# Kernel tuning notes

Hardware: AMD Instinct MI355X
Metric: run time of the kernel (lower is better)

Reference implementation:

```python
import jax, jax.numpy as jnp
import numpy as np

T, B, XD, HD, ZD = 256, 512, 64, 512, 32
EPS_C = 1e-5  # EPS in the torch source

SHAPES = {
    "x": (T, B, XD), "eps": (T, B, ZD),
    "phi_x_W1": (HD, XD), "phi_x_b1": (HD,), "phi_x_W2": (HD, HD), "phi_x_b2": (HD,),
    "phi_z_W": (HD, ZD), "phi_z_b": (HD,),
    "enc_W1": (HD, 2 * HD), "enc_b1": (HD,), "enc_W2": (HD, HD), "enc_b2": (HD,),
    "enc_mean_W": (ZD, HD), "enc_mean_b": (ZD,), "enc_std_W": (ZD, HD), "enc_std_b": (ZD,),
    "prior_W": (HD, HD), "prior_b": (HD,),
    "prior_mean_W": (ZD, HD), "prior_mean_b": (ZD,), "prior_std_W": (ZD, HD), "prior_std_b": (ZD,),
    "dec_W1": (HD, 2 * HD), "dec_b1": (HD,), "dec_W2": (HD, HD), "dec_b2": (HD,),
    "dec_std_W": (XD, HD), "dec_std_b": (XD,),
    "dec_mean_W1": (XD, HD), "dec_mean_b1": (XD,), "dec_mean_W2": (XD, XD), "dec_mean_b2": (XD,),
    "gru_Wih": (3 * HD, 2 * HD), "gru_Whh": (3 * HD, HD),
}

def setup_inputs() -> dict:
    key = jax.random.key(0)
    out = {}
    for i, (name, shp) in enumerate(SHAPES.items()):
        scale = 1.0 if name in ("x", "eps") else 0.05
        out[name] = jax.random.normal(jax.random.fold_in(key, i), shp, jnp.float32) * scale
    return out

def _lin(x, W, b):
    return x @ W.T + b

def _vrnn(x, eps, p):
    relu, softplus, sigmoid = jax.nn.relu, jax.nn.softplus, jax.nn.sigmoid
    h0 = jnp.zeros((x.shape[1], HD), x.dtype)  # n_layers = 1

    def step(h, xe):
        xt, et = xe  # [B, XD], [B, ZD]
        phi_x = relu(_lin(relu(_lin(xt, p["phi_x_W1"], p["phi_x_b1"])), p["phi_x_W2"], p["phi_x_b2"]))
        enc_h = relu(_lin(relu(_lin(jnp.concatenate([phi_x, h], 1), p["enc_W1"], p["enc_b1"])), p["enc_W2"], p["enc_b2"]))
        enc_mean = _lin(enc_h, p["enc_mean_W"], p["enc_mean_b"])
        enc_std = softplus(_lin(enc_h, p["enc_std_W"], p["enc_std_b"]))
        prior_h = relu(_lin(h, p["prior_W"], p["prior_b"]))
        prior_mean = _lin(prior_h, p["prior_mean_W"], p["prior_mean_b"])
        prior_std = softplus(_lin(prior_h, p["prior_std_W"], p["prior_std_b"]))
        z = et * enc_std + enc_mean  # reparameterized sample with pre-drawn eps
        z = z.at[:, :4].multiply(10.0)  # _modify_z(modify_dims=[0,1,2,3], scale=10, shift=0)
        phi_z = relu(_lin(z, p["phi_z_W"], p["phi_z_b"]))
        dec_h = relu(_lin(relu(_lin(jnp.concatenate([phi_z, h], 1), p["dec_W1"], p["dec_b1"])), p["dec_W2"], p["dec_b2"]))
        dec_mean = _lin(relu(_lin(dec_h, p["dec_mean_W1"], p["dec_mean_b1"])), p["dec_mean_W2"], p["dec_mean_b2"])
        dec_std = softplus(_lin(dec_h, p["dec_std_W"], p["dec_std_b"]))
        # single-layer GRU cell, no bias (PyTorch gate order: r, z, n)
        gx = jnp.concatenate([phi_x, phi_z], 1) @ p["gru_Wih"].T
        gh = h @ p["gru_Whh"].T
        xr, xz, xn = jnp.split(gx, 3, 1)
        hr, hz, hn = jnp.split(gh, 3, 1)
        r = sigmoid(xr + hr)
        zg = sigmoid(xz + hz)
        n = jnp.tanh(xn + r * hn)
        h_new = (1.0 - zg) * n + zg * h
        s1 = jnp.maximum(enc_std, 1e-9)
        s2 = jnp.maximum(prior_std, 1e-9)
        kld = 0.5 * jnp.sum(jnp.log(s2 ** 2 / s1 ** 2) + (s1 ** 2 + (enc_mean - prior_mean) ** 2) / s2 ** 2 - 1.0)
        nll = jnp.sum(jnp.log(dec_std + EPS_C) + jnp.log(2.0 * jnp.pi) / 2.0 + (xt - dec_mean) ** 2 / (2.0 * dec_std ** 2))
        return h_new, (dec_mean, kld, nll)

    _, (dec_means, klds, nlls) = jax.lax.scan(step, h0, (x, eps))
    rec_loss = jnp.sum((dec_means - x) ** 2)  # F.mse_loss(..., reduction='sum')
    return rec_loss, jnp.sum(klds), jnp.sum(nlls), dec_means

def reference(x, eps, phi_x_W1, phi_x_b1, phi_x_W2, phi_x_b2, phi_z_W, phi_z_b, enc_W1, enc_b1, enc_W2, enc_b2, enc_mean_W, enc_mean_b, enc_std_W, enc_std_b, prior_W, prior_b, prior_mean_W, prior_mean_b, prior_std_W, prior_std_b, dec_W1, dec_b1, dec_W2, dec_b2, dec_std_W, dec_std_b, dec_mean_W1, dec_mean_b1, dec_mean_W2, dec_mean_b2, gru_Wih, gru_Whh):
    args = dict(locals())
    xv = args.pop("x")
    ev = args.pop("eps")
    return _vrnn(xv, ev, args)
```

## Files before the change

kernel.cpp:

```cpp
#include <hip/hip_runtime.h>
#include <hip/hip_bf16.h>
#include <math.h>


typedef __attribute__((ext_vector_type(8))) short bfrag;
typedef __attribute__((ext_vector_type(4))) short sfrag;
typedef __attribute__((ext_vector_type(4))) float ffrag;
typedef __hip_bfloat16 bf16;

__device__ __forceinline__ float softplus_f(float v) {
    return (v > 20.f) ? v : log1pf(expf(v));
}
__device__ __forceinline__ float sigmoid_f(float v) {
    return 1.f / (1.f + expf(-v));
}
__device__ __forceinline__ float s2f(short s) {
    union { unsigned u; float f; } c;
    c.u = ((unsigned)(unsigned short)s) << 16;
    return c.f;
}

__global__ __launch_bounds__(256) void f2b_kernel(
    const float* __restrict__ s, bf16* __restrict__ d, int n)
{
    int i = blockIdx.x * 256 + threadIdx.x;
    if (i < n) d[i] = __float2bfloat16(s[i]);
}
__global__ __launch_bounds__(256) void fcopy_kernel(
    const float* __restrict__ s, float* __restrict__ d, int n)
{
    int i = blockIdx.x * 256 + threadIdx.x;
    if (i < n) d[i] = s[i];
}

__global__ __launch_bounds__(256) void packw_kernel(
    const float* __restrict__ src, bf16* __restrict__ dst,
    int ldw, int n0, int k0, int KB, int total)
{
    int i = blockIdx.x * 256 + threadIdx.x;
    if (i >= total) return;
    const int j = i & 7;
    const int L = (i >> 3) & 63;
    const int r = i >> 9;
    const int kb = r % KB, t = r / KB;
    dst[i] = __float2bfloat16(
        src[(size_t)(n0 + t * 16 + (L & 15)) * ldw + k0 + kb * 32 + ((L >> 4) * 8) + j]);
}

__global__ __launch_bounds__(256) void init_kernel(
    float* __restrict__ hlive, bf16* __restrict__ hh0, float* __restrict__ out)
{
    const int idx = blockIdx.x * 256 + threadIdx.x;
    if (idx < 262144) { hlive[idx] = 0.f; hh0[idx] = __float2bfloat16(0.f); }
    if (idx < 3) out[idx] = 0.f;
}

__global__ __launch_bounds__(256) void gemm_p(
    const bf16* __restrict__ A0, int lda0, const bf16* __restrict__ W0p, int K0,
    const bf16* __restrict__ A1, int lda1, const bf16* __restrict__ W1p, int K1,
    const float* __restrict__ bias, int act,
    void* __restrict__ C, int ldc, int obf)
{
    __shared__ __align__(16) bf16 As[2][64][72];
    const int tid = threadIdx.x;
    const int L = tid & 63, w = tid >> 6;
    const int m0 = blockIdx.y * 64;
    const int n0 = blockIdx.x * 64;
    const int lr = L & 15, lk = (L >> 4) * 8;
    const int msub = (w & 1) * 32, nsub = (w >> 1) * 32;
    const int srow = tid >> 2, scol = (tid & 3) * 16;
    const size_t Lo = (size_t)L * 8;

    ffrag acc[2][2];
#pragma unroll
    for (int i = 0; i < 2; ++i)
#pragma unroll
        for (int j = 0; j < 2; ++j)
#pragma unroll
            for (int r = 0; r < 4; ++r) acc[i][j][r] = 0.f;

    for (int s = 0; s < 2; ++s) {
        const bf16* A = s ? A1 : A0;
        if (!A) break;
        const bf16* Wp = s ? W1p : W0p;
        const int lda = s ? lda1 : lda0;
        const int K   = s ? K1 : K0;
        const int KB = K >> 5;
        const int NP = K >> 6;
        const size_t t0 = (size_t)((n0 + nsub) >> 4);

        {
            const bf16* ap = A + (size_t)(m0 + srow) * lda + scol;
            *(bfrag*)&As[0][srow][scol]     = *(const bfrag*)(ap);
            *(bfrag*)&As[0][srow][scol + 8] = *(const bfrag*)(ap + 8);
        }
        __syncthreads();

        for (int kp = 0; kp < NP; ++kp) {
            if (kp + 1 < NP) {
                const bf16* ap = A + (size_t)(m0 + srow) * lda + (kp + 1) * 64 + scol;
                bf16* dst = &As[(kp + 1) & 1][srow][scol];
                *(bfrag*)(dst)     = *(const bfrag*)(ap);
                *(bfrag*)(dst + 8) = *(const bfrag*)(ap + 8);
            }
#pragma unroll
            for (int kbi = 0; kbi < 2; ++kbi) {
                const int kb = kp * 2 + kbi;
                bfrag b0 = *(const bfrag*)(Wp + ((t0 * KB + kb) << 9) + Lo);
                bfrag b1 = *(const bfrag*)(Wp + (((t0 + 1) * KB + kb) << 9) + Lo);
                bfrag a0 = *(const bfrag*)&As[kp & 1][msub + lr][kbi * 32 + lk];
                bfrag a1 = *(const bfrag*)&As[kp & 1][msub + 16 + lr][kbi * 32 + lk];
                acc[0][0] = __builtin_amdgcn_mfma_f32_16x16x32_bf16(a0, b0, acc[0][0], 0, 0, 0);
                acc[0][1] = __builtin_amdgcn_mfma_f32_16x16x32_bf16(a0, b1, acc[0][1], 0, 0, 0);
                acc[1][0] = __builtin_amdgcn_mfma_f32_16x16x32_bf16(a1, b0, acc[1][0], 0, 0, 0);
                acc[1][1] = __builtin_amdgcn_mfma_f32_16x16x32_bf16(a1, b1, acc[1][1], 0, 0, 0);
            }
            __syncthreads();
        }
    }

#pragma unroll
    for (int i = 0; i < 2; ++i)
#pragma unroll
    for (int j = 0; j < 2; ++j)
#pragma unroll
    for (int r = 0; r < 4; ++r) {
        const int row = m0 + msub + 16 * i + (L >> 4) * 4 + r;
        const int col = n0 + nsub + 16 * j + lr;
        float v = acc[i][j][r];
        if (bias) v += bias[col];
        if (act == 1) v = fmaxf(v, 0.f);
        else if (act == 2) { if (col >= 32) v = softplus_f(v); }
        else if (act == 3) { if (col < 64) v = fmaxf(v, 0.f); }
        if (obf == 1) {
            ((bf16*)C)[(size_t)row * ldc + col] = __float2bfloat16(v);
        } else if (obf == 2) {
            ((bf16*)C)[((size_t)(row >> 4) * (ldc >> 4) + (col >> 4)) * 256
                       + (size_t)L * 4 + r] = __float2bfloat16(v);
        } else {
            ((float*)C)[(size_t)row * ldc + col] = v;
        }
    }
}

#define AST 536

__global__ __launch_bounds__(512, 1) void encmid_kernel(
    const bf16* __restrict__ e1xp,
    const float* __restrict__ eps_c,
    const bf16* __restrict__ ew1hp,
    const bf16* __restrict__ ew2p,
    const float* __restrict__ eb2,
    const bf16* __restrict__ mswp,
    const float* __restrict__ msb,
    const bf16* __restrict__ pzwp,
    const float* __restrict__ pzb,
    bf16* __restrict__ hh,
    float* __restrict__ emsc,
    bf16* __restrict__ phizc,
    bf16* __restrict__ pzp,
    bf16* __restrict__ hpp,
    int lt, int hsrc0)
{
    __shared__ __align__(16) bf16 hB[16][AST];
    __shared__ __align__(16) bf16 p1[16][AST];
    __shared__ __align__(16) bf16 p2[16][AST];
    __shared__ float msd[16][65];
    __shared__ __align__(16) bf16 zb[16][40];

    const int tid = threadIdx.x;
    const int L = tid & 63, w = tid >> 6;
    const int lr = L & 15, lk = (L >> 4) * 8;
    const int rq = (L >> 4) * 4;
    const int bm = blockIdx.x;
    const int m0 = bm * 16;

    const int hrow = tid >> 5, hc0 = (tid & 31) * 16;
    const size_t Lo = (size_t)L * 8;

    const size_t rb = (size_t)lt * 512 + m0;
    const size_t rt = (size_t)lt * 32 + bm;

    {
        const int slot = (lt == 0) ? hsrc0 : lt;
        const bf16* hsv = hh + (size_t)slot * 262144 + (size_t)(m0 + hrow) * 512 + hc0;
        bfrag h0 = *(const bfrag*)(hsv);
        bfrag h1 = *(const bfrag*)(hsv + 8);
        *(bfrag*)&hB[hrow][hc0]     = h0;
        *(bfrag*)&hB[hrow][hc0 + 8] = h1;
        if (lt == 0 && hsrc0 != 0) {
            bf16* d0 = hh + (size_t)(m0 + hrow) * 512 + hc0;
            *(bfrag*)(d0)     = h0;
            *(bfrag*)(d0 + 8) = h1;
        }
    }
    __syncthreads();

#pragma unroll
    for (int q = 0; q < 2; ++q) {
        const int kb = w * 2 + q;
        *(bfrag*)(hpp + (((size_t)bm * 16 + kb) << 9) + Lo) =
            *(const bfrag*)&hB[lr][kb * 32 + lk];
    }

    {
        sfrag exv[4];
#pragma unroll
        for (int nt = 0; nt < 4; ++nt)
            exv[nt] = *(const sfrag*)(e1xp + (rt * 32 + 4 * w + nt) * 256 + (size_t)L * 4);

        bfrag wf[4][4];
#pragma unroll
        for (int d = 0; d < 4; ++d)
#pragma unroll
            for (int nt = 0; nt < 4; ++nt)
                wf[d][nt] = *(const bfrag*)(ew1hp + (((4 * w + nt) * 16 + d) << 9) + Lo);

        ffrag acc[4];
#pragma unroll
        for (int nt = 0; nt < 4; ++nt)
#pragma unroll
            for (int r = 0; r < 4; ++r) acc[nt][r] = 0.f;

#pragma unroll
        for (int kb = 0; kb < 16; ++kb) {
            bfrag a = *(const bfrag*)&hB[lr][kb * 32 + lk];
            const int cur = kb & 3;
#pragma unroll
            for (int nt = 0; nt < 4; ++nt)
                acc[nt] = __builtin_amdgcn_mfma_f32_16x16x32_bf16(a, wf[cur][nt], acc[nt], 0, 0, 0);
            if (kb < 12)
#pragma unroll
                for (int nt = 0; nt < 4; ++nt)
                    wf[cur][nt] = *(const bfrag*)(ew1hp + (((4 * w + nt) * 16 + kb + 4) << 9) + Lo);
        }
#pragma unroll
        for (int nt = 0; nt < 4; ++nt)
#pragma unroll
        for (int r = 0; r < 4; ++r) {
            const int row = rq + r, col = 64 * w + 16 * nt + lr;
            float v = acc[nt][r] + s2f(exv[nt][r]);
            p1[row][col] = __float2bfloat16(fmaxf(v, 0.f));
        }
    }
    __syncthreads();

    {
        bfrag wf[4][4];
#pragma unroll
        for (int d = 0; d < 4; ++d)
#pragma unroll
            for (int nt = 0; nt < 4; ++nt)
                wf[d][nt] = *(const bfrag*)(ew2p + (((4 * w + nt) * 16 + d) << 9) + Lo);

        ffrag acc[4];
#pragma unroll
        for (int nt = 0; nt < 4; ++nt)
#pragma unroll
            for (int r = 0; r < 4; ++r) acc[nt][r] = 0.f;

#pragma unroll
        for (int kb = 0; kb < 16; ++kb) {
            bfrag a = *(const bfrag*)&p1[lr][kb * 32 + lk];
            const int cur = kb & 3;
#pragma unroll
            for (int nt = 0; nt < 4; ++nt)
                acc[nt] = __builtin_amdgcn_mfma_f32_16x16x32_bf16(a, wf[cur][nt], acc[nt], 0, 0, 0);
            if (kb < 12)
#pragma unroll
                for (int nt = 0; nt < 4; ++nt)
                    wf[cur][nt] = *(const bfrag*)(ew2p + (((4 * w + nt) * 16 + kb + 4) << 9) + Lo);
        }
#pragma unroll
        for (int nt = 0; nt < 4; ++nt)
#pragma unroll
        for (int r = 0; r < 4; ++r) {
            const int row = rq + r, col = 64 * w + 16 * nt + lr;
            float v = fmaxf(acc[nt][r] + eb2[col], 0.f);
            p2[row][col] = __float2bfloat16(v);
        }
    }
    __syncthreads();

    if (w < 4) {
        bfrag mf[4];
#pragma unroll
        for (int d = 0; d < 4; ++d)
            mf[d] = *(const bfrag*)(mswp + ((w * 16 + d) << 9) + Lo);
        ffrag acc;
#pragma unroll
        for (int r = 0; r < 4; ++r) acc[r] = 0.f;
#pragma unroll
        for (int kb = 0; kb < 16; ++kb) {
            bfrag a = *(const bfrag*)&p2[lr][kb * 32 + lk];
            const int cur = kb & 3;
            acc = __builtin_amdgcn_mfma_f32_16x16x32_bf16(a, mf[cur], acc, 0, 0, 0);
            if (kb < 12)
                mf[cur] = *(const bfrag*)(mswp + ((w * 16 + kb + 4) << 9) + Lo);
        }
#pragma unroll
        for (int r = 0; r < 4; ++r) {
            const int row = rq + r, col = 16 * w + lr;
            float v = acc[r] + msb[col];
            if (col >= 32) v = softplus_f(v);
            msd[row][col] = v;
            emsc[(rb + row) * 64 + col] = v;
        }
    }
    __syncthreads();

    {
        const int row = tid >> 5, c = tid & 31;
        float zv = eps_c[(rb + row) * 32 + c] * msd[row][32 + c] + msd[row][c];
        if (c < 4) zv *= 10.f;
        zb[row][c] = __float2bfloat16(zv);
    }
    __syncthreads();

    {
        bfrag a = *(const bfrag*)&zb[lr][lk];
#pragma unroll
        for (int nt = 0; nt < 4; ++nt) {
            const int col = 64 * w + 16 * nt + lr;
            bfrag b = *(const bfrag*)(pzwp + ((4 * w + nt) << 9) + Lo);
            ffrag c_;
#pragma unroll
            for (int r = 0; r < 4; ++r) c_[r] = 0.f;
            c_ = __builtin_amdgcn_mfma_f32_16x16x32_bf16(a, b, c_, 0, 0, 0);
#pragma unroll
            for (int r = 0; r < 4; ++r) {
                const int row = rq + r;
                const float v = fmaxf(c_[r] + pzb[col], 0.f);
                p1[row][col] = __float2bfloat16(v);
            }
        }
    }
    __syncthreads();

#pragma unroll
    for (int q = 0; q < 2; ++q) {
        const int kb = w * 2 + q;
        *(bfrag*)(pzp + (((size_t)bm * 16 + kb) << 9) + Lo) =
            *(const bfrag*)&p1[lr][kb * 32 + lk];
    }
    {
        const int prow = tid >> 5, pc0 = (tid & 31) * 16;
        bf16* pp = phizc + (rb + prow) * 512 + pc0;
        *(bfrag*)(pp)     = *(const bfrag*)&p1[prow][pc0];
        *(bfrag*)(pp + 8) = *(const bfrag*)&p1[prow][pc0 + 8];
    }
}

__global__ __launch_bounds__(256) void gru_kernel(
    const bf16* __restrict__ gxxp,
    const bf16* __restrict__ wihzp,
    const bf16* __restrict__ whhp,
    const bf16* __restrict__ pzp,
    const bf16* __restrict__ hpp,
    float* __restrict__ hlive,
    bf16* __restrict__ hnx,
    int lt)
{
    const int tid = threadIdx.x;
    const int L = tid & 63, w = tid >> 6;
    const int lr = L & 15;
    const int rq = (L >> 4) * 4;
    const int jt = blockIdx.x;
    const int rt = blockIdx.y * 4 + w;
    const size_t Lo = (size_t)L * 8;

    bfrag wz[2][3], wh[2][3], az2[2], ah2[2];
#pragma unroll
    for (int q = 0; q < 2; ++q) {
#pragma unroll
        for (int g = 0; g < 3; ++g) {
            wz[q][g] = *(const bfrag*)(wihzp + (((size_t)(jt + 32 * g) * 16 + q) << 9) + Lo);
            wh[q][g] = *(const bfrag*)(whhp  + (((size_t)(jt + 32 * g) * 16 + q) << 9) + Lo);
        }
        az2[q] = *(const bfrag*)(pzp + (((size_t)rt * 16 + q) << 9) + Lo);
        ah2[q] = *(const bfrag*)(hpp + (((size_t)rt * 16 + q) << 9) + Lo);
    }

    ffrag sR, sZ, aN, hN;
#pragma unroll
    for (int r = 0; r < 4; ++r) { sR[r] = 0.f; sZ[r] = 0.f; aN[r] = 0.f; hN[r] = 0.f; }

#pragma unroll
    for (int kb = 0; kb < 16; ++kb) {
        const int cur = kb & 1;
        sR = __builtin_amdgcn_mfma_f32_16x16x32_bf16(az2[cur], wz[cur][0], sR, 0, 0, 0);
        sR = __builtin_amdgcn_mfma_f32_16x16x32_bf16(ah2[cur], wh[cur][0], sR, 0, 0, 0);
        sZ = __builtin_amdgcn_mfma_f32_16x16x32_bf16(az2[cur], wz[cur][1], sZ, 0, 0, 0);
        sZ = __builtin_amdgcn_mfma_f32_16x16x32_bf16(ah2[cur], wh[cur][1], sZ, 0, 0, 0);
        aN = __builtin_amdgcn_mfma_f32_16x16x32_bf16(az2[cur], wz[cur][2], aN, 0, 0, 0);
        hN = __builtin_amdgcn_mfma_f32_16x16x32_bf16(ah2[cur], wh[cur][2], hN, 0, 0, 0);
        if (kb < 14) {
#pragma unroll
            for (int g = 0; g < 3; ++g) {
                wz[cur][g] = *(const bfrag*)(wihzp + (((size_t)(jt + 32 * g) * 16 + kb + 2) << 9) + Lo);
                wh[cur][g] = *(const bfrag*)(whhp  + (((size_t)(jt + 32 * g) * 16 + kb + 2) << 9) + Lo);
            }
            az2[cur] = *(const bfrag*)(pzp + (((size_t)rt * 16 + kb + 2) << 9) + Lo);
            ah2[cur] = *(const bfrag*)(hpp + (((size_t)rt * 16 + kb + 2) << 9) + Lo);
        }
    }

    const size_t gb = ((size_t)lt * 32 + rt) * 96;
    sfrag gr = *(const sfrag*)(gxxp + (gb + jt     ) * 256 + (size_t)L * 4);
    sfrag gz = *(const sfrag*)(gxxp + (gb + jt + 32) * 256 + (size_t)L * 4);
    sfrag gn = *(const sfrag*)(gxxp + (gb + jt + 64) * 256 + (size_t)L * 4);
    const int colg = jt * 16 + lr;
#pragma unroll
    for (int r = 0; r < 4; ++r) {
        const int row = rt * 16 + rq + r;
        const size_t gidx = (size_t)row * 512 + colg;
        const float rg = sigmoid_f(s2f(gr[r]) + sR[r]);
        const float zg = sigmoid_f(s2f(gz[r]) + sZ[r]);
        const float nv = tanhf(s2f(gn[r]) + aN[r] + rg * hN[r]);
        const float hv = hlive[gidx];
        const float hnew = (1.f - zg) * nv + zg * hv;
        hlive[gidx] = hnew;
        hnx[gidx] = __float2bfloat16(hnew);
    }
}

__global__ __launch_bounds__(256) void kld_kernel(
    const float* __restrict__ emsc, const float* __restrict__ pms,
    float* __restrict__ out)
{
    const size_t p0 = (size_t)blockIdx.x * 1024 + threadIdx.x;
    float acc = 0.f;
#pragma unroll
    for (int rep = 0; rep < 4; ++rep) {
        const size_t p = p0 + (size_t)rep * 256;
        const size_t i = p >> 5; const int c = p & 31;
        const float m1 = emsc[i * 64 + c];
        const float s1 = fmaxf(emsc[i * 64 + 32 + c], 1e-9f);
        const float m2 = pms[i * 64 + c];
        const float s2 = fmaxf(pms[i * 64 + 32 + c], 1e-9f);
        const float dm = m1 - m2;
        acc += 2.f * (logf(s2) - logf(s1)) + (s1 * s1 + dm * dm) / (s2 * s2) - 1.f;
    }
    for (int off = 32; off > 0; off >>= 1) acc += __shfl_down(acc, off);
    __shared__ float tmp[4];
    if ((threadIdx.x & 63) == 0) tmp[threadIdx.x >> 6] = acc;
    __syncthreads();
    if (threadIdx.x == 0)
        atomicAdd(out + 1, 0.5f * (tmp[0] + tmp[1] + tmp[2] + tmp[3]));
}

__global__ __launch_bounds__(256) void final_kernel(
    const float* __restrict__ ddc,
    const float* __restrict__ W2,
    const float* __restrict__ b2,
    const float* __restrict__ x,
    float* __restrict__ sums,
    float* __restrict__ outDM)
{
    __shared__ float Dh[32][64];
    __shared__ float W2s[64][65];
    const int tid = threadIdx.x;
    const size_t r0 = (size_t)blockIdx.x * 32;

    for (int i = tid; i < 32 * 64; i += 256)
        Dh[i >> 6][i & 63] = ddc[(r0 + (i >> 6)) * 128 + (i & 63)];
    for (int i = tid; i < 64 * 64; i += 256) W2s[i >> 6][i & 63] = W2[i];
    __syncthreads();

    float rec = 0.f, nll = 0.f;
#pragma unroll
    for (int rep = 0; rep < 8; ++rep) {
        const int idx = rep * 256 + tid;
        const int r = idx >> 6, j = idx & 63;
        float acc = b2[j];
#pragma unroll 8
        for (int k = 0; k < 64; ++k) acc += Dh[r][k] * W2s[j][k];
        const size_t g = (r0 + r) * 64 + j;
        const float xv = x[g];
        const float sd = softplus_f(ddc[(r0 + r) * 128 + 64 + j]);
        outDM[g] = acc;
        const float d = xv - acc;
        rec += d * d;
        nll += logf(sd + 1e-5f) + 0.9189385332046727f + d * d / (2.f * sd * sd);
    }
    for (int off = 32; off > 0; off >>= 1) {
        rec += __shfl_down(rec, off);
        nll += __shfl_down(nll, off);
    }
    __shared__ float rr[4], nn[4];
    if ((tid & 63) == 0) { rr[tid >> 6] = rec; nn[tid >> 6] = nll; }
    __syncthreads();
    if (tid == 0) {
        atomicAdd(sums + 0, rr[0] + rr[1] + rr[2] + rr[3]);
        atomicAdd(sums + 2, nn[0] + nn[1] + nn[2] + nn[3]);
    }
}


static void gp(hipStream_t s, int M, int N,
               const bf16* A0, int lda0, const bf16* W0p, int K0,
               const bf16* A1, int lda1, const bf16* W1p, int K1,
               const float* bias, int act, void* C, int ldc, int obf)
{
    dim3 g(N / 64, M / 64), b(256);
    hipLaunchKernelGGL(gemm_p, g, b, 0, s,
                       A0, lda0, W0p, K0, A1, lda1, W1p, K1,
                       bias, act, C, ldc, obf);
}

static void f2b(hipStream_t s, const float* src, bf16* dst, int n) {
    hipLaunchKernelGGL(f2b_kernel, dim3((n + 255) / 256), dim3(256), 0, s, src, dst, n);
}
static void fcp(hipStream_t s, const float* src, float* dst, int n) {
    hipLaunchKernelGGL(fcopy_kernel, dim3((n + 255) / 256), dim3(256), 0, s, src, dst, n);
}
static void packw(hipStream_t s, const float* src, __hip_bfloat16* dst,
                  int ldw, int n0, int k0, int KB, int total) {
    hipLaunchKernelGGL(packw_kernel, dim3((total + 255) / 256), dim3(256), 0, s,
                       src, dst, ldw, n0, k0, KB, total);
}

#define P_EW1H 0
#define P_EW2  262144
#define P_MSW  524288
#define P_PZW  557056
#define P_WIHZ 573440
#define P_WHH  1359872
#define P_PXW1 2146304
#define P_PXW2 2179072
#define P_EW1X 2441216
#define P_WIHX 2703360
#define P_PRW  3489792
#define P_PMS  3751936
#define P_DW1Z 3784704
#define P_DW1H 4046848
#define P_DW2  4308992
#define P_DDW  4571136

static size_t ws_needed(int tc) {
    size_t off = 28148736ull + (size_t)(tc + 1) * 524288ull;
    off += (size_t)tc * 524288ull;
    off += (size_t)tc * 524288ull;
    off += (size_t)tc * 524288ull;
    off += (size_t)tc * 131072ull;
    off += (size_t)tc * 262144ull;
    off += (size_t)tc * 1572864ull;
    return off;
}

extern "C" void kernel_launch(void* const* d_in, const int* in_sizes, int n_in,
                              void* d_out, int out_size, void* d_ws, size_t ws_size,
                              hipStream_t stream)
{
    const float* x_in   = (const float*)d_in[0];
    const float* eps_in = (const float*)d_in[1];
    const float* pxW1 = (const float*)d_in[2];  const float* pxb1 = (const float*)d_in[3];
    const float* pxW2 = (const float*)d_in[4];  const float* pxb2 = (const float*)d_in[5];
    const float* pzW  = (const float*)d_in[6];  const float* pzb  = (const float*)d_in[7];
    const float* eW1  = (const float*)d_in[8];  const float* eb1  = (const float*)d_in[9];
    const float* eW2  = (const float*)d_in[10]; const float* eb2  = (const float*)d_in[11];
    const float* emW  = (const float*)d_in[12]; const float* emb  = (const float*)d_in[13];
    const float* esW  = (const float*)d_in[14]; const float* esb  = (const float*)d_in[15];
    const float* prW  = (const float*)d_in[16]; const float* prb  = (const float*)d_in[17];
    const float* pmW  = (const float*)d_in[18]; const float* pmb  = (const float*)d_in[19];
    const float* psW  = (const float*)d_in[20]; const float* psb  = (const float*)d_in[21];
    const float* dW1  = (const float*)d_in[22]; const float* db1  = (const float*)d_in[23];
    const float* dW2  = (const float*)d_in[24]; const float* db2  = (const float*)d_in[25];
    const float* dsW  = (const float*)d_in[26]; const float* dsb  = (const float*)d_in[27];
    const float* dmW1 = (const float*)d_in[28]; const float* dmb1 = (const float*)d_in[29];
    const float* dmW2 = (const float*)d_in[30]; const float* dmb2 = (const float*)d_in[31];
    const float* gWih = (const float*)d_in[32]; const float* gWhh = (const float*)d_in[33];

    float* out = (float*)d_out;
    char* ws = (char*)d_ws;

    int TC = 1;
    const int cands[9] = {256, 128, 64, 32, 16, 8, 4, 2, 1};
    for (int i = 0; i < 9; ++i)
        if (ws_needed(cands[i]) <= ws_size) { TC = cands[i]; break; }
    const int NCH = 256 / TC;

    bf16*  WPK   = (bf16*)(ws);
    float* BB    = (float*)(ws + 9273344ull);
    bf16*  XBF   = (bf16*)(ws + 9274368ull);
    float* HLIVE = (float*)(ws + 26051584ull);
    bf16*  PZP   = (bf16*)(ws + 27100160ull);
    bf16*  HPP   = (bf16*)(ws + 27624448ull);
    bf16*  HH    = (bf16*)(ws + 28148736ull);
    size_t off = 28148736ull + (size_t)(TC + 1) * 524288ull;
    bf16*  R1    = (bf16*)(ws + off); off += (size_t)TC * 524288ull;
    bf16*  R2    = (bf16*)(ws + off); off += (size_t)TC * 524288ull;
    bf16*  PHIZC = (bf16*)(ws + off); off += (size_t)TC * 524288ull;
    float* EMSC  = (float*)(ws + off); off += (size_t)TC * 131072ull;
    float* U     = (float*)(ws + off); off += (size_t)TC * 262144ull;
    bf16*  GXX   = (bf16*)(ws + off);

    f2b(stream, x_in, XBF, 8388608);
    fcp(stream, emb,  BB + 0,   32);
    fcp(stream, esb,  BB + 32,  32);
    fcp(stream, pmb,  BB + 64,  32);
    fcp(stream, psb,  BB + 96,  32);
    fcp(stream, dmb1, BB + 128, 64);
    fcp(stream, dsb,  BB + 192, 64);

    packw(stream, eW1,  WPK + P_EW1H, 1024, 0, 512, 16, 262144);
    packw(stream, eW2,  WPK + P_EW2,   512, 0,   0, 16, 262144);
    packw(stream, emW,  WPK + P_MSW,   512, 0,   0, 16, 16384);
    packw(stream, esW,  WPK + P_MSW + 16384, 512, 0, 0, 16, 16384);
    packw(stream, pzW,  WPK + P_PZW,    32, 0,   0,  1, 16384);
    packw(stream, gWih, WPK + P_WIHZ, 1024, 0, 512, 16, 786432);
    packw(stream, gWhh, WPK + P_WHH,   512, 0,   0, 16, 786432);
    packw(stream, pxW1, WPK + P_PXW1,   64, 0,   0,  2, 32768);
    packw(stream, pxW2, WPK + P_PXW2,  512, 0,   0, 16, 262144);
    packw(stream, eW1,  WPK + P_EW1X, 1024, 0,   0, 16, 262144);
    packw(stream, gWih, WPK + P_WIHX, 1024, 0,   0, 16, 786432);
    packw(stream, prW,  WPK + P_PRW,   512, 0,   0, 16, 262144);
    packw(stream, pmW,  WPK + P_PMS,   512, 0,   0, 16, 16384);
    packw(stream, psW,  WPK + P_PMS + 16384, 512, 0, 0, 16, 16384);
    packw(stream, dW1,  WPK + P_DW1Z, 1024, 0,   0, 16, 262144);
    packw(stream, dW1,  WPK + P_DW1H, 1024, 0, 512, 16, 262144);
    packw(stream, dW2,  WPK + P_DW2,   512, 0,   0, 16, 262144);
    packw(stream, dmW1, WPK + P_DDW,   512, 0,   0, 16, 32768);
    packw(stream, dsW,  WPK + P_DDW + 32768, 512, 0, 0, 16, 32768);

    hipLaunchKernelGGL(init_kernel, dim3(1024), dim3(256), 0, stream,
                       HLIVE, HH, out);

    for (int c = 0; c < NCH; ++c) {
        const int cs = c * TC;
        const int MR = TC * 512;

        gp(stream, MR, 512, XBF + (size_t)cs * 32768, 64, WPK + P_PXW1, 64,
           nullptr, 0, nullptr, 0, pxb1, 1, R1, 512, 1);
        gp(stream, MR, 512, R1, 512, WPK + P_PXW2, 512,
           nullptr, 0, nullptr, 0, pxb2, 1, R2, 512, 1);

        gp(stream, MR, 512, R2, 512, WPK + P_EW1X, 512,
           nullptr, 0, nullptr, 0, eb1, 0, R1, 512, 2);
        gp(stream, MR, 1536, R2, 512, WPK + P_WIHX, 512,
           nullptr, 0, nullptr, 0, nullptr, 0, GXX, 1536, 2);

        for (int lt = 0; lt < TC; ++lt) {
            hipLaunchKernelGGL(encmid_kernel, dim3(32), dim3(512), 0, stream,
                               R1, eps_in + (size_t)cs * 16384,
                               WPK + P_EW1H, WPK + P_EW2, eb2,
                               WPK + P_MSW, BB, WPK + P_PZW, pzb,
                               HH, EMSC, PHIZC, PZP, HPP,
                               lt, (c == 0) ? 0 : TC);
            hipLaunchKernelGGL(gru_kernel, dim3(32, 8), dim3(256), 0, stream,
                               GXX, WPK + P_WIHZ, WPK + P_WHH, PZP, HPP,
                               HLIVE, HH + (size_t)(lt + 1) * 262144, lt);
        }

        gp(stream, MR, 512, HH, 512, WPK + P_PRW, 512,
           nullptr, 0, nullptr, 0, prb, 1, R1, 512, 1);
        gp(stream, MR, 64, R1, 512, WPK + P_PMS, 512,
           nullptr, 0, nullptr, 0, BB + 64, 2, U, 64, 0);
        hipLaunchKernelGGL(kld_kernel, dim3(TC * 16), dim3(256), 0, stream,
                           EMSC, U, out);

        gp(stream, MR, 512, PHIZC, 512, WPK + P_DW1Z, 512,
           HH, 512, WPK + P_DW1H, 512, db1, 1, R1, 512, 1);
        gp(stream, MR, 512, R1, 512, WPK + P_DW2, 512,
           nullptr, 0, nullptr, 0, db2, 1, R2, 512, 1);
        gp(stream, MR, 128, R2, 512, WPK + P_DDW, 512,
           nullptr, 0, nullptr, 0, BB + 128, 3, U, 128, 0);
        hipLaunchKernelGGL(final_kernel, dim3(MR / 32), dim3(256), 0, stream,
                           U, dmW2, dmb2, x_in + (size_t)cs * 32768,
                           out, out + 3 + (size_t)cs * 32768);
    }
}
```

Baseline: 8.799 ms.

## Fuse GRU update into per-step encoder kernel and add nontemporal memory hints

Folds the GRU gate computation into the per-timestep encoder kernel, which becomes step_kernel. The phi_z and h tiles are read straight from shared memory, so the PZP/HPP staging buffers and one kernel launch per timestep go away. The price is that the GRU work now runs on only 32 blocks instead of 256, with each wave handling four column tiles in sequence and streaming the full GRU weights. Streaming activations (gate inputs, eps, enc outputs, phi_z) also switch to nontemporal loads and stores to reduce cache pollution.

```diff
diff --git a/kernel.cpp b/kernel.cpp
--- a/kernel.cpp
+++ b/kernel.cpp
@@ -18,6 +18,18 @@
     union { unsigned u; float f; } c;
     c.u = ((unsigned)(unsigned short)s) << 16;
     return c.f;
+}
+__device__ __forceinline__ sfrag ntl4(const bf16* p) {
+    return __builtin_nontemporal_load((const sfrag*)p);
+}
+__device__ __forceinline__ void nts8(bf16* p, bfrag v) {
+    __builtin_nontemporal_store(v, (bfrag*)p);
+}
+__device__ __forceinline__ float ntlf(const float* p) {
+    return __builtin_nontemporal_load(p);
+}
+__device__ __forceinline__ void ntsf(float* p, float v) {
+    __builtin_nontemporal_store(v, p);
 }
 
 __global__ __launch_bounds__(256) void f2b_kernel(
@@ -145,8 +157,9 @@
 
 #define AST 536
 
-__global__ __launch_bounds__(512, 1) void encmid_kernel(
+__global__ __launch_bounds__(512, 1) void step_kernel(
     const bf16* __restrict__ e1xp,
+    const bf16* __restrict__ gxxp,
     const float* __restrict__ eps_c,
     const bf16* __restrict__ ew1hp,
     const bf16* __restrict__ ew2p,
@@ -155,11 +168,12 @@
     const float* __restrict__ msb,
     const bf16* __restrict__ pzwp,
     const float* __restrict__ pzb,
+    const bf16* __restrict__ wihzp,
+    const bf16* __restrict__ whhp,
+    float* __restrict__ hlive,
     bf16* __restrict__ hh,
     float* __restrict__ emsc,
     bf16* __restrict__ phizc,
-    bf16* __restrict__ pzp,
-    bf16* __restrict__ hpp,
     int lt, int hsrc0)
 {
     __shared__ __align__(16) bf16 hB[16][AST];
@@ -196,18 +210,11 @@
     }
     __syncthreads();
 
-#pragma unroll
-    for (int q = 0; q < 2; ++q) {
-        const int kb = w * 2 + q;
-        *(bfrag*)(hpp + (((size_t)bm * 16 + kb) << 9) + Lo) =
-            *(const bfrag*)&hB[lr][kb * 32 + lk];
-    }
-
     {
         sfrag exv[4];
 #pragma unroll
         for (int nt = 0; nt < 4; ++nt)
-            exv[nt] = *(const sfrag*)(e1xp + (rt * 32 + 4 * w + nt) * 256 + (size_t)L * 4);
+            exv[nt] = ntl4(e1xp + (rt * 32 + 4 * w + nt) * 256 + (size_t)L * 4);
 
         bfrag wf[4][4];
 #pragma unroll
@@ -304,14 +311,14 @@
             float v = acc[r] + msb[col];
             if (col >= 32) v = softplus_f(v);
             msd[row][col] = v;
-            emsc[(rb + row) * 64 + col] = v;
+            ntsf(&emsc[(rb + row) * 64 + col], v);
         }
     }
     __syncthreads();
 
     {
         const int row = tid >> 5, c = tid & 31;
-        float zv = eps_c[(rb + row) * 32 + c] * msd[row][32 + c] + msd[row][c];
+        float zv = ntlf(&eps_c[(rb + row) * 32 + c]) * msd[row][32 + c] + msd[row][c];
         if (c < 4) zv *= 10.f;
         zb[row][c] = __float2bfloat16(zv);
     }
@@ -337,90 +344,78 @@
     }
     __syncthreads();
 
-#pragma unroll
-    for (int q = 0; q < 2; ++q) {
-        const int kb = w * 2 + q;
-        *(bfrag*)(pzp + (((size_t)bm * 16 + kb) << 9) + Lo) =
-            *(const bfrag*)&p1[lr][kb * 32 + lk];
-    }
     {
         const int prow = tid >> 5, pc0 = (tid & 31) * 16;
         bf16* pp = phizc + (rb + prow) * 512 + pc0;
-        *(bfrag*)(pp)     = *(const bfrag*)&p1[prow][pc0];
-        *(bfrag*)(pp + 8) = *(const bfrag*)&p1[prow][pc0 + 8];
-    }
-}
-
-__global__ __launch_bounds__(256) void gru_kernel(
-    const bf16* __restrict__ gxxp,
-    const bf16* __restrict__ wihzp,
-    const bf16* __restrict__ whhp,
-    const bf16* __restrict__ pzp,
-    const bf16* __restrict__ hpp,
-    float* __restrict__ hlive,
-    bf16* __restrict__ hnx,
-    int lt)
-{
-    const int tid = threadIdx.x;
-    const int L = tid & 63, w = tid >> 6;
-    const int lr = L & 15;
-    const int rq = (L >> 4) * 4;
-    const int jt = blockIdx.x;
-    const int rt = blockIdx.y * 4 + w;
-    const size_t Lo = (size_t)L * 8;
-
-    bfrag wz[2][3], wh[2][3], az2[2], ah2[2];
-#pragma unroll
-    for (int q = 0; q < 2; ++q) {
-#pragma unroll
-        for (int g = 0; g < 3; ++g) {
-            wz[q][g] = *(const bfrag*)(wihzp + (((size_t)(jt + 32 * g) * 16 + q) << 9) + Lo);
-            wh[q][g] = *(const bfrag*)(whhp  + (((size_t)(jt + 32 * g) * 16 + q) << 9) + Lo);
-        }
-        az2[q] = *(const bfrag*)(pzp + (((size_t)rt * 16 + q) << 9) + Lo);
-        ah2[q] = *(const bfrag*)(hpp + (((size_t)rt * 16 + q) << 9) + Lo);
-    }
-
-    ffrag sR, sZ, aN, hN;
-#pragma unroll
-    for (int r = 0; r < 4; ++r) { sR[r] = 0.f; sZ[r] = 0.f; aN[r] = 0.f; hN[r] = 0.f; }
-
-#pragma unroll
-    for (int kb = 0; kb < 16; ++kb) {
-        const int cur = kb & 1;
-        sR = __builtin_amdgcn_mfma_f32_16x16x32_bf16(az2[cur], wz[cur][0], sR, 0, 0, 0);
-        sR = __builtin_amdgcn_mfma_f32_16x16x32_bf16(ah2[cur], wh[cur][0], sR, 0, 0, 0);
-        sZ = __builtin_amdgcn_mfma_f32_16x16x32_bf16(az2[cur], wz[cur][1], sZ, 0, 0, 0);
-        sZ = __builtin_amdgcn_mfma_f32_16x16x32_bf16(ah2[cur], wh[cur][1], sZ, 0, 0, 0);
-        aN = __builtin_amdgcn_mfma_f32_16x16x32_bf16(az2[cur], wz[cur][2], aN, 0, 0, 0);
-        hN = __builtin_amdgcn_mfma_f32_16x16x32_bf16(ah2[cur], wh[cur][2], hN, 0, 0, 0);
-        if (kb < 14) {
-#pragma unroll
-            for (int g = 0; g < 3; ++g) {
-                wz[cur][g] = *(const bfrag*)(wihzp + (((size_t)(jt + 32 * g) * 16 + kb + 2) << 9) + Lo);
-                wh[cur][g] = *(const bfrag*)(whhp  + (((size_t)(jt + 32 * g) * 16 + kb + 2) << 9) + Lo);
+        nts8(pp,     *(const bfrag*)&p1[prow][pc0]);
+        nts8(pp + 8, *(const bfrag*)&p1[prow][pc0 + 8]);
+    }
+
+    {
+        bf16* hnx = hh + (size_t)(lt + 1) * 262144;
+
+        sfrag gr[4], gz[4], gn[4];
+        float hvp[4][4];
+#pragma unroll
+        for (int nt = 0; nt < 4; ++nt) {
+            const int jt = 4 * w + nt;
+            gr[nt] = ntl4(gxxp + (rt * 96 + jt     ) * 256 + (size_t)L * 4);
+            gz[nt] = ntl4(gxxp + (rt * 96 + jt + 32) * 256 + (size_t)L * 4);
+            gn[nt] = ntl4(gxxp + (rt * 96 + jt + 64) * 256 + (size_t)L * 4);
+#pragma unroll
+            for (int r = 0; r < 4; ++r)
+                hvp[nt][r] = hlive[(size_t)(m0 + rq + r) * 512 + jt * 16 + lr];
+        }
+
+#pragma unroll
+        for (int nt = 0; nt < 4; ++nt) {
+            const int jt = 4 * w + nt;
+
+            bfrag wz[2][3], wh[2][3];
+#pragma unroll
+            for (int q = 0; q < 2; ++q)
+#pragma unroll
+                for (int g = 0; g < 3; ++g) {
+                    wz[q][g] = *(const bfrag*)(wihzp + (((size_t)(jt + 32 * g) * 16 + q) << 9) + Lo);
+                    wh[q][g] = *(const bfrag*)(whhp  + (((size_t)(jt + 32 * g) * 16 + q) << 9) + Lo);
+                }
+
+            ffrag sR, sZ, aN, hN;
+#pragma unroll
+            for (int r = 0; r < 4; ++r) { sR[r] = 0.f; sZ[r] = 0.f; aN[r] = 0.f; hN[r] = 0.f; }
+
+#pragma unroll
+            for (int kb = 0; kb < 16; ++kb) {
+                const int cur = kb & 1;
+                bfrag aZ = *(const bfrag*)&p1[lr][kb * 32 + lk];
+                bfrag aH = *(const bfrag*)&hB[lr][kb * 32 + lk];
+                sR = __builtin_amdgcn_mfma_f32_16x16x32_bf16(aZ, wz[cur][0], sR, 0, 0, 0);
+                sR = __builtin_amdgcn_mfma_f32_16x16x32_bf16(aH, wh[cur][0], sR, 0, 0, 0);
+                sZ = __builtin_amdgcn_mfma_f32_16x16x32_bf16(aZ, wz[cur][1], sZ, 0, 0, 0);
+                sZ = __builtin_amdgcn_mfma_f32_16x16x32_bf16(aH, wh[cur][1], sZ, 0, 0, 0);
+                aN = __builtin_amdgcn_mfma_f32_16x16x32_bf16(aZ, wz[cur][2], aN, 0, 0, 0);
+                hN = __builtin_amdgcn_mfma_f32_16x16x32_bf16(aH, wh[cur][2], hN, 0, 0, 0);
+                if (kb < 14)
+#pragma unroll
+                    for (int g = 0; g < 3; ++g) {
+                        wz[cur][g] = *(const bfrag*)(wihzp + (((size_t)(jt + 32 * g) * 16 + kb + 2) << 9) + Lo);
+                        wh[cur][g] = *(const bfrag*)(whhp  + (((size_t)(jt + 32 * g) * 16 + kb + 2) << 9) + Lo);
+                    }
             }
-            az2[cur] = *(const bfrag*)(pzp + (((size_t)rt * 16 + kb + 2) << 9) + Lo);
-            ah2[cur] = *(const bfrag*)(hpp + (((size_t)rt * 16 + kb + 2) << 9) + Lo);
-        }
-    }
-
-    const size_t gb = ((size_t)lt * 32 + rt) * 96;
-    sfrag gr = *(const sfrag*)(gxxp + (gb + jt     ) * 256 + (size_t)L * 4);
-    sfrag gz = *(const sfrag*)(gxxp + (gb + jt + 32) * 256 + (size_t)L * 4);
-    sfrag gn = *(const sfrag*)(gxxp + (gb + jt + 64) * 256 + (size_t)L * 4);
-    const int colg = jt * 16 + lr;
-#pragma unroll
-    for (int r = 0; r < 4; ++r) {
-        const int row = rt * 16 + rq + r;
-        const size_t gidx = (size_t)row * 512 + colg;
-        const float rg = sigmoid_f(s2f(gr[r]) + sR[r]);
-        const float zg = sigmoid_f(s2f(gz[r]) + sZ[r]);
-        const float nv = tanhf(s2f(gn[r]) + aN[r] + rg * hN[r]);
-        const float hv = hlive[gidx];
-        const float hnew = (1.f - zg) * nv + zg * hv;
-        hlive[gidx] = hnew;
-        hnx[gidx] = __float2bfloat16(hnew);
+
+#pragma unroll
+            for (int r = 0; r < 4; ++r) {
+                const int row = rq + r;
+                const int col = jt * 16 + lr;
+                const size_t gidx = (size_t)(m0 + row) * 512 + col;
+                const float rg = sigmoid_f(s2f(gr[nt][r]) + sR[r]);
+                const float zg = sigmoid_f(s2f(gz[nt][r]) + sZ[r]);
+                const float nv = tanhf(s2f(gn[nt][r]) + aN[r] + rg * hN[r]);
+                const float hnew = (1.f - zg) * nv + zg * hvp[nt][r];
+                hlive[gidx] = hnew;
+                hnx[gidx] = __float2bfloat16(hnew);
+            }
+        }
     }
 }
 
@@ -538,7 +533,7 @@
 #define P_DDW  4571136
 
 static size_t ws_needed(int tc) {
-    size_t off = 28148736ull + (size_t)(tc + 1) * 524288ull;
+    size_t off = 27100160ull + (size_t)(tc + 1) * 524288ull;
     off += (size_t)tc * 524288ull;
     off += (size_t)tc * 524288ull;
     off += (size_t)tc * 524288ull;
@@ -584,10 +579,8 @@
     float* BB    = (float*)(ws + 9273344ull);
     bf16*  XBF   = (bf16*)(ws + 9274368ull);
     float* HLIVE = (float*)(ws + 26051584ull);
-    bf16*  PZP   = (bf16*)(ws + 27100160ull);
-    bf16*  HPP   = (bf16*)(ws + 27624448ull);
-    bf16*  HH    = (bf16*)(ws + 28148736ull);
-    size_t off = 28148736ull + (size_t)(TC + 1) * 524288ull;
+    bf16*  HH    = (bf16*)(ws + 27100160ull);
+    size_t off = 27100160ull + (size_t)(TC + 1) * 524288ull;
     bf16*  R1    = (bf16*)(ws + off); off += (size_t)TC * 524288ull;
     bf16*  R2    = (bf16*)(ws + off); off += (size_t)TC * 524288ull;
     bf16*  PHIZC = (bf16*)(ws + off); off += (size_t)TC * 524288ull;
@@ -641,15 +634,13 @@
            nullptr, 0, nullptr, 0, nullptr, 0, GXX, 1536, 2);
 
         for (int lt = 0; lt < TC; ++lt) {
-            hipLaunchKernelGGL(encmid_kernel, dim3(32), dim3(512), 0, stream,
-                               R1, eps_in + (size_t)cs * 16384,
+            hipLaunchKernelGGL(step_kernel, dim3(32), dim3(512), 0, stream,
+                               R1, GXX, eps_in + (size_t)cs * 16384,
                                WPK + P_EW1H, WPK + P_EW2, eb2,
                                WPK + P_MSW, BB, WPK + P_PZW, pzb,
-                               HH, EMSC, PHIZC, PZP, HPP,
+                               WPK + P_WIHZ, WPK + P_WHH,
+                               HLIVE, HH, EMSC, PHIZC,
                                lt, (c == 0) ? 0 : TC);
-            hipLaunchKernelGGL(gru_kernel, dim3(32, 8), dim3(256), 0, stream,
-                               GXX, WPK + P_WIHZ, WPK + P_WHH, PZP, HPP,
-                               HLIVE, HH + (size_t)(lt + 1) * 262144, lt);
         }
 
         gp(stream, MR, 512, HH, 512, WPK + P_PRW, 512,
```

Result: slower. 16.50 ms (+87.5%).

## Add 128x128-tile GEMM variant with double-buffered A and per-wave 64x64 subtiles

Applied to the files above, without the earlier changes.

Adds a gemm_p2 kernel that computes 128x128 output tiles, where each of four waves owns a 64x64 subtile with a 4x4 MFMA accumulator grid. The A operand is staged through double-buffered shared memory, and the pre-packed weights are read straight from global memory. The launcher uses it whenever M and N are multiples of 128 and keeps the old 64x64 kernel otherwise. The larger tile raises operand reuse per load. In exchange it means fewer blocks, lower occupancy and higher register pressure from 64 accumulator floats per lane.

```diff
diff --git a/kernel.cpp b/kernel.cpp
--- a/kernel.cpp
+++ b/kernel.cpp
@@ -128,6 +128,102 @@
         const int row = m0 + msub + 16 * i + (L >> 4) * 4 + r;
         const int col = n0 + nsub + 16 * j + lr;
         float v = acc[i][j][r];
+        if (bias) v += bias[col];
+        if (act == 1) v = fmaxf(v, 0.f);
+        else if (act == 2) { if (col >= 32) v = softplus_f(v); }
+        else if (act == 3) { if (col < 64) v = fmaxf(v, 0.f); }
+        if (obf == 1) {
+            ((bf16*)C)[(size_t)row * ldc + col] = __float2bfloat16(v);
+        } else if (obf == 2) {
+            ((bf16*)C)[((size_t)(row >> 4) * (ldc >> 4) + (col >> 4)) * 256
+                       + (size_t)L * 4 + r] = __float2bfloat16(v);
+        } else {
+            ((float*)C)[(size_t)row * ldc + col] = v;
+        }
+    }
+}
+
+__global__ __launch_bounds__(256) void gemm_p2(
+    const bf16* __restrict__ A0, int lda0, const bf16* __restrict__ W0p, int K0,
+    const bf16* __restrict__ A1, int lda1, const bf16* __restrict__ W1p, int K1,
+    const float* __restrict__ bias, int act,
+    void* __restrict__ C, int ldc, int obf)
+{
+    __shared__ __align__(16) bf16 As[2][128][72];
+    const int tid = threadIdx.x;
+    const int L = tid & 63, w = tid >> 6;
+    const int m0 = blockIdx.y * 128;
+    const int n0 = blockIdx.x * 128;
+    const int lr = L & 15, lk = (L >> 4) * 8;
+    const int wr = (w & 1) * 64, wc = (w >> 1) * 64;
+    const int srow = tid >> 1, scol = (tid & 1) * 32;
+    const size_t Lo = (size_t)L * 8;
+
+    ffrag acc[4][4];
+#pragma unroll
+    for (int m = 0; m < 4; ++m)
+#pragma unroll
+        for (int n = 0; n < 4; ++n)
+#pragma unroll
+            for (int r = 0; r < 4; ++r) acc[m][n][r] = 0.f;
+
+    for (int s = 0; s < 2; ++s) {
+        const bf16* A = s ? A1 : A0;
+        if (!A) break;
+        const bf16* Wp = s ? W1p : W0p;
+        const int lda = s ? lda1 : lda0;
+        const int K   = s ? K1 : K0;
+        const int KB = K >> 5;
+        const int NP = K >> 6;
+        const size_t t0 = (size_t)((n0 + wc) >> 4);
+
+        {
+            const bf16* ap = A + (size_t)(m0 + srow) * lda + scol;
+            *(bfrag*)&As[0][srow][scol]      = *(const bfrag*)(ap);
+            *(bfrag*)&As[0][srow][scol + 8]  = *(const bfrag*)(ap + 8);
+            *(bfrag*)&As[0][srow][scol + 16] = *(const bfrag*)(ap + 16);
+            *(bfrag*)&As[0][srow][scol + 24] = *(const bfrag*)(ap + 24);
+        }
+        __syncthreads();
+
+        for (int kp = 0; kp < NP; ++kp) {
+            if (kp + 1 < NP) {
+                const bf16* ap = A + (size_t)(m0 + srow) * lda + (kp + 1) * 64 + scol;
+                bf16* dst = &As[(kp + 1) & 1][srow][scol];
+                *(bfrag*)(dst)      = *(const bfrag*)(ap);
+                *(bfrag*)(dst + 8)  = *(const bfrag*)(ap + 8);
+                *(bfrag*)(dst + 16) = *(const bfrag*)(ap + 16);
+                *(bfrag*)(dst + 24) = *(const bfrag*)(ap + 24);
+            }
+#pragma unroll
+            for (int kbi = 0; kbi < 2; ++kbi) {
+                const int kb = kp * 2 + kbi;
+                bfrag bf[4], af[4];
+#pragma unroll
+                for (int n = 0; n < 4; ++n)
+                    bf[n] = *(const bfrag*)(Wp + (((t0 + n) * KB + kb) << 9) + Lo);
+#pragma unroll
+                for (int m = 0; m < 4; ++m)
+                    af[m] = *(const bfrag*)&As[kp & 1][wr + m * 16 + lr][kbi * 32 + lk];
+#pragma unroll
+                for (int m = 0; m < 4; ++m)
+#pragma unroll
+                    for (int n = 0; n < 4; ++n)
+                        acc[m][n] = __builtin_amdgcn_mfma_f32_16x16x32_bf16(af[m], bf[n], acc[m][n], 0, 0, 0);
+            }
+            __syncthreads();
+        }
+    }
+
+#pragma unroll
+    for (int m = 0; m < 4; ++m)
+#pragma unroll
+    for (int n = 0; n < 4; ++n)
+#pragma unroll
+    for (int r = 0; r < 4; ++r) {
+        const int row = m0 + wr + m * 16 + (L >> 4) * 4 + r;
+        const int col = n0 + wc + n * 16 + lr;
+        float v = acc[m][n][r];
         if (bias) v += bias[col];
         if (act == 1) v = fmaxf(v, 0.f);
         else if (act == 2) { if (col >= 32) v = softplus_f(v); }
@@ -502,10 +598,17 @@
                const bf16* A1, int lda1, const bf16* W1p, int K1,
                const float* bias, int act, void* C, int ldc, int obf)
 {
-    dim3 g(N / 64, M / 64), b(256);
-    hipLaunchKernelGGL(gemm_p, g, b, 0, s,
-                       A0, lda0, W0p, K0, A1, lda1, W1p, K1,
-                       bias, act, C, ldc, obf);
+    if ((N & 127) == 0 && (M & 127) == 0) {
+        dim3 g(N / 128, M / 128), b(256);
+        hipLaunchKernelGGL(gemm_p2, g, b, 0, s,
+                           A0, lda0, W0p, K0, A1, lda1, W1p, K1,
+                           bias, act, C, ldc, obf);
+    } else {
+        dim3 g(N / 64, M / 64), b(256);
+        hipLaunchKernelGGL(gemm_p, g, b, 0, s,
+                           A0, lda0, W0p, K0, A1, lda1, W1p, K1,
+                           bias, act, C, ldc, obf);
+    }
 }
 
 static void f2b(hipStream_t s, const float* src, bf16* dst, int n) {
```

After: 9.328 ms. 6.0% more time.
